# Kernel optimization log

Hardware: AMD Instinct MI355X
Metric: run time of the kernel (lower is better)

Reference implementation:

```python
import jax, jax.numpy as jnp
import numpy as np

HIDDEN, HEADS, HDIM = 1024, 8, 64
B, S = 4, 8192
LN_EPS = 1e-6


def setup_inputs() -> dict:
    key = jax.random.key(0)
    ks = jax.random.split(key, 12)
    inner = HEADS * HDIM
    sd = HIDDEN ** -0.5
    return {
        "x": jax.random.normal(ks[0], (B, S, HIDDEN), jnp.float32),
        "Wq": jax.random.normal(ks[1], (HIDDEN, inner), jnp.float32) * sd,
        "bq": jnp.zeros((inner,), jnp.float32),
        "Wk": jax.random.normal(ks[2], (HIDDEN, inner), jnp.float32) * sd,
        "bk": jnp.zeros((inner,), jnp.float32),
        "Wv": jax.random.normal(ks[3], (HIDDEN, inner), jnp.float32) * sd,
        "bv": jnp.zeros((inner,), jnp.float32),
        "Wo": jax.random.normal(ks[4], (inner, HIDDEN), jnp.float32) * (inner ** -0.5),
        "bo": jnp.zeros((HIDDEN,), jnp.float32),
        "alpha": jnp.ones((HEADS, HDIM), jnp.float32),
        "aug_param": jax.random.normal(ks[5], (1, HEADS, HDIM), jnp.float32),
        "ln_scale": jnp.ones((HIDDEN,), jnp.float32),
        "ln_bias": jnp.zeros((HIDDEN,), jnp.float32),
    }


def reference(x, Wq, bq, Wk, bk, Wv, bv, Wo, bo, alpha, aug_param, ln_scale, ln_bias):
    b, s, _ = x.shape
    h, d = alpha.shape
    scale = d ** -0.5
    q = (x @ Wq + bq).reshape(b, s, h, d)
    k = (x @ Wk + bk).reshape(b, s, h, d)
    v = (x @ Wv + bv).reshape(b, s, h, d)
    decay = jax.nn.sigmoid(alpha)  # (h, d)

    def step(state, qkv):
        q_t, k_t, v_t = qkv  # each (b, h, d)
        attn = jax.nn.softmax(jnp.einsum('bhd,bhd->bh', q_t, k_t) * scale, axis=-1)
        new_state = decay * state + (1.0 - decay) * attn[..., None] * v_t
        return new_state, new_state

    qs = jnp.moveaxis(q, 1, 0)  # (s, b, h, d)
    ks_ = jnp.moveaxis(k, 1, 0)
    vs = jnp.moveaxis(v, 1, 0)
    init = jnp.zeros((b, h, d), x.dtype)
    _, states = jax.lax.scan(step, init, (qs, ks_, vs))
    states = jnp.moveaxis(states, 0, 1)  # (b, s, h, d)

    aug = jax.nn.sigmoid(q * aug_param)  # aug_param (1,h,d) broadcasts over (b,s,h,d)
    out = (q * states + aug).reshape(b, s, h * d)
    out = out @ Wo + bo
    mean = jnp.mean(out, axis=-1, keepdims=True)
    var = jnp.var(out, axis=-1, keepdims=True)
    return (out - mean) * jax.lax.rsqrt(var + LN_EPS) * ln_scale + ln_bias
```

## Files before the change

kernel.cpp:

```cpp
#include <hip/hip_runtime.h>
#include <hip/hip_bf16.h>


#define HIDDEN 1024
#define HEADS 8
#define HDIM 64
#define INNER 512
#define BATCH 4
#define SEQ 8192
#define ROWS (BATCH*SEQ)
#define NCHUNK 128
#define CHLEN 64

typedef unsigned short u16;
typedef unsigned int u32;
typedef __attribute__((ext_vector_type(8))) short bf16x8;
typedef __attribute__((ext_vector_type(4))) float f32x4;

__device__ __forceinline__ float b2f(u16 u) { return __uint_as_float(((u32)u) << 16); }
__device__ __forceinline__ u16 f2b(float f) {
  u32 u = __float_as_uint(f);
  u32 r = u + 0x7fffu + ((u >> 16) & 1u);
  return (u16)(r >> 16);
}
__device__ __forceinline__ u32 pack2(float a, float b) {
  return (u32)f2b(a) | ((u32)f2b(b) << 16);
}

#define GLOAD_LDS16(gp, lp)                                                  \
  __builtin_amdgcn_global_load_lds(                                          \
      (const __attribute__((address_space(1))) u32*)(gp),                    \
      (__attribute__((address_space(3))) u32*)(lp), 16, 0, 0)

__global__ __launch_bounds__(256) void prep_x(const float* __restrict__ x,
                                              u16* __restrict__ xb) {
  size_t i = ((size_t)blockIdx.x * 256 + threadIdx.x) * 8;
  float4 a = *(const float4*)(x + i);
  float4 b = *(const float4*)(x + i + 4);
  uint4 w = {pack2(a.x, a.y), pack2(a.z, a.w), pack2(b.x, b.y), pack2(b.z, b.w)};
  *(uint4*)(xb + i) = w;
}

__global__ __launch_bounds__(256) void prep_w(
    const float* __restrict__ Wq, const float* __restrict__ Wk,
    const float* __restrict__ Wv, const float* __restrict__ Wo,
    const float* __restrict__ bq, const float* __restrict__ bk,
    const float* __restrict__ bv,
    u16* __restrict__ Wt, u16* __restrict__ Wot, float* __restrict__ bcat) {
  const int WELEM = HIDDEN * INNER;
  int idx = blockIdx.x * 256 + threadIdx.x;
  if (idx < 3 * WELEM) {
    int z = idx / WELEM;
    int rem = idx - z * WELEM;
    int n = rem >> 10;
    int k = rem & 1023;
    const float* W = (z == 0) ? Wq : (z == 1) ? Wk : Wv;
    Wt[idx] = f2b(W[k * INNER + n]);
  } else {
    int rem = idx - 3 * WELEM;
    int n = rem >> 9;
    int k = rem & 511;
    Wot[rem] = f2b(Wo[k * HIDDEN + n]);
  }
  if (idx < 3 * INNER) {
    int z = idx >> 9;
    int n = idx & 511;
    bcat[idx] = (z == 0) ? bq[n] : (z == 1) ? bk[n] : bv[n];
  }
}

template <int K, bool SPLIT3>
__global__ __launch_bounds__(512, 2) void gemm_8ph(
    const u16* __restrict__ A, const u16* __restrict__ Bt,
    const float* __restrict__ bias,
    void* __restrict__ out0, void* __restrict__ out1, void* __restrict__ out2,
    int nTilesN) {
  constexpr int NT = K / 32;
  __shared__ u16 lds[4][16384];

  const int nwg = gridDim.x;
  const int chunk = nwg >> 3;
  const int bid = blockIdx.x;
  const int lin = (bid & 7) * chunk + (bid >> 3);
  const int nt = lin % nTilesN;
  const int mt = lin / nTilesN;
  const int m0 = mt * 256, n0 = nt * 256;
  const int N = nTilesN * 256;

  const int tid = threadIdx.x;
  const int lane = tid & 63;
  const int w = tid >> 6;
  const int wm = w >> 2;
  const int wn = w & 3;
  const int r16 = lane & 15, kq = lane >> 4;

  const int rt = tid >> 2;
  const int cg = (((tid & 3) << 3)) ^ (((rt >> 1) & 3) << 3);
  const u16* Ag = A + (size_t)(m0 + rt) * K + cg;
  const u16* Bg = Bt + (size_t)(n0 + rt) * K + cg;
  const int ldst = w * 512;

#define STAGE_A(slot, kt)                                                     \
  {                                                                           \
    GLOAD_LDS16(Ag + (size_t)(kt) * 32, &lds[slot][ldst]);                    \
    GLOAD_LDS16(Ag + (size_t)(kt) * 32 + (size_t)128 * K,                     \
                &lds[slot][4096 + ldst]);                                     \
  }
#define STAGE_B(slot, kt)                                                     \
  {                                                                           \
    GLOAD_LDS16(Bg + (size_t)(kt) * 32, &lds[slot][8192 + ldst]);             \
    GLOAD_LDS16(Bg + (size_t)(kt) * 32 + (size_t)128 * K,                     \
                &lds[slot][12288 + ldst]);                                    \
  }

  const int xk = (kq << 3) ^ (((r16 >> 1) & 3) << 3);
  const int aO = (wm * 128 + r16) * 32 + xk;
  const int bO = 8192 + (wn * 64 + r16) * 32 + xk;

  f32x4 acc[8][4] = {};
  bf16x8 af[4], bfv[4];

#define PH0(t_, STG)                                                           \
  {                                                                            \
    const u16* sl = &lds[(t_) & 3][0];                                         \
    _Pragma("unroll") for (int i = 0; i < 4; i++)                              \
        af[i] = *(const bf16x8*)&sl[aO + i * 512];                             \
    _Pragma("unroll") for (int j = 0; j < 4; j++)                              \
        bfv[j] = *(const bf16x8*)&sl[bO + j * 512];                            \
    STG;                                                                       \
    __builtin_amdgcn_sched_barrier(0);                                         \
    __builtin_amdgcn_s_barrier();                                              \
    asm volatile("s_waitcnt lgkmcnt(0)" ::: "memory");                         \
    __builtin_amdgcn_sched_barrier(0);                                         \
    __builtin_amdgcn_s_setprio(1);                                             \
    _Pragma("unroll") for (int i = 0; i < 4; i++)                              \
        _Pragma("unroll") for (int j = 0; j < 4; j++)                          \
            acc[i][j] =                                                        \
        __builtin_amdgcn_mfma_f32_16x16x32_bf16(af[i], bfv[j], acc[i][j], 0, 0, 0); \
    __builtin_amdgcn_s_setprio(0);                                             \
    __builtin_amdgcn_sched_barrier(0);                                         \
    __builtin_amdgcn_s_barrier();                                              \
  }

#define PH1(t_, STG, VM)                                                       \
  {                                                                            \
    const u16* sl = &lds[(t_) & 3][0];                                         \
    _Pragma("unroll") for (int i = 0; i < 4; i++)                              \
        af[i] = *(const bf16x8*)&sl[aO + (i + 4) * 512];                       \
    STG;                                                                       \
    asm volatile("s_waitcnt vmcnt(" #VM ")" ::: "memory");                     \
    __builtin_amdgcn_sched_barrier(0);                                         \
    __builtin_amdgcn_s_barrier();                                              \
    asm volatile("s_waitcnt lgkmcnt(0)" ::: "memory");                         \
    __builtin_amdgcn_sched_barrier(0);                                         \
    __builtin_amdgcn_s_setprio(1);                                             \
    _Pragma("unroll") for (int i = 0; i < 4; i++)                              \
        _Pragma("unroll") for (int j = 0; j < 4; j++)                          \
            acc[i + 4][j] =                                                    \
        __builtin_amdgcn_mfma_f32_16x16x32_bf16(af[i], bfv[j], acc[i + 4][j], 0, 0, 0); \
    __builtin_amdgcn_s_setprio(0);                                             \
    __builtin_amdgcn_sched_barrier(0);                                         \
    __builtin_amdgcn_s_barrier();                                              \
  }

#define NOSTG ((void)0)

  STAGE_A(0, 0); STAGE_B(0, 0);
  STAGE_A(1, 1); STAGE_B(1, 1);
  STAGE_A(2, 2); STAGE_B(2, 2);
  asm volatile("s_waitcnt vmcnt(8)" ::: "memory");
  __builtin_amdgcn_sched_barrier(0);
  __builtin_amdgcn_s_barrier();

  for (int t = 0; t < NT - 3; ++t) {
    PH0(t, STAGE_A((t + 3) & 3, t + 3));
    PH1(t, STAGE_B((t + 3) & 3, t + 3), 8);
  }
  PH0(NT - 3, NOSTG);
  PH1(NT - 3, NOSTG, 4);
  PH0(NT - 2, NOSTG);
  PH1(NT - 2, NOSTG, 0);
  PH0(NT - 1, NOSTG);
  PH1(NT - 1, NOSTG, 0);
#undef PH0
#undef PH1
#undef NOSTG
#undef STAGE_A
#undef STAGE_B

  float* fl = (float*)(&lds[0][0]) + w * 4096;
  const int zsel = SPLIT3 ? ((n0 + wn * 64) >> 9) : 0;
  u16* ob = SPLIT3 ? (u16*)((zsel == 0) ? out0 : (zsel == 1) ? out1 : out2)
                   : (u16*)out0;
  const int OC = SPLIT3 ? INNER : N;
  const int colloc = (lane & 7) * 8;
  const int gcol = (SPLIT3 ? ((n0 + wn * 64) & 511) : (n0 + wn * 64)) + colloc;
  const int lrowr = lane >> 3;
  float bvj[4];
#pragma unroll
  for (int j = 0; j < 4; j++) bvj[j] = bias[n0 + wn * 64 + j * 16 + r16];

#pragma unroll
  for (int pass = 0; pass < 4; ++pass) {
#pragma unroll
    for (int ii = 0; ii < 2; ++ii) {
#pragma unroll
      for (int j = 0; j < 4; ++j) {
#pragma unroll
        for (int q = 0; q < 4; ++q)
          fl[(ii * 16 + kq * 4 + q) * 68 + j * 16 + r16] =
              acc[pass * 2 + ii][j][q] + bvj[j];
      }
    }
#pragma unroll
    for (int inst = 0; inst < 4; ++inst) {
      int lr = inst * 8 + lrowr;
      float4 f0 = *(float4*)&fl[lr * 68 + colloc];
      float4 f1 = *(float4*)&fl[lr * 68 + colloc + 4];
      uint4 wv = {pack2(f0.x, f0.y), pack2(f0.z, f0.w),
                  pack2(f1.x, f1.y), pack2(f1.z, f1.w)};
      size_t grow = (size_t)(m0 + wm * 128 + pass * 32 + lr);
      *(uint4*)&ob[grow * OC + gcol] = wv;
    }
  }
}

template <bool A_BF16>
__global__ __launch_bounds__(256) void gemm128(
    const void* __restrict__ Aany, const u16* __restrict__ BtBase,
    const float* __restrict__ bias0, const float* __restrict__ bias1,
    const float* __restrict__ bias2,
    void* __restrict__ out0, void* __restrict__ out1, void* __restrict__ out2,
    int K) {
  __shared__ u16 As[128 * 32];
  __shared__ u16 Bs[128 * 32];
  const int N = gridDim.x * 128;
  const int z = blockIdx.z;
  const u16* Bt = BtBase + (size_t)z * N * K;
  const float* bias = (z == 0) ? bias0 : (z == 1) ? bias1 : bias2;
  void* Out = (z == 0) ? out0 : (z == 1) ? out1 : out2;
  const int tid = threadIdx.x;
  const int m0 = blockIdx.y * 128;
  const int n0 = blockIdx.x * 128;
  const int lane = tid & 63;
  const int wid = tid >> 6;
  const int wm = wid >> 1, wn = wid & 1;
  const int r16 = lane & 15, kq = lane >> 4;
  const int r = tid >> 1;
  const int half = tid & 1;
  f32x4 acc[4][4] = {};
  for (int k0 = 0; k0 < K; k0 += 32) {
    __syncthreads();
    if (A_BF16) {
      const u16* Ab = (const u16*)Aany;
      const int4* src = (const int4*)(Ab + (size_t)(m0 + r) * K + k0 + half * 16);
      int4 v0 = src[0];
      int4 v1 = src[1];
      *(int4*)&As[r * 32 + half * 16] = v0;
      *(int4*)&As[r * 32 + half * 16 + 8] = v1;
    } else {
      const float* Af = (const float*)Aany;
      const float4* src = (const float4*)(Af + (size_t)(m0 + r) * K + k0 + half * 16);
      float4 f0 = src[0], f1 = src[1], f2 = src[2], f3 = src[3];
      uint4 w0 = {pack2(f0.x, f0.y), pack2(f0.z, f0.w), pack2(f1.x, f1.y), pack2(f1.z, f1.w)};
      uint4 w1 = {pack2(f2.x, f2.y), pack2(f2.z, f2.w), pack2(f3.x, f3.y), pack2(f3.z, f3.w)};
      *(uint4*)&As[r * 32 + half * 16] = w0;
      *(uint4*)&As[r * 32 + half * 16 + 8] = w1;
    }
    {
      const int4* src = (const int4*)(Bt + (size_t)(n0 + r) * K + k0 + half * 16);
      int4 v0 = src[0];
      int4 v1 = src[1];
      *(int4*)&Bs[r * 32 + half * 16] = v0;
      *(int4*)&Bs[r * 32 + half * 16 + 8] = v1;
    }
    __syncthreads();
    bf16x8 a[4], b[4];
#pragma unroll
    for (int i = 0; i < 4; i++)
      a[i] = *(const bf16x8*)&As[(wm * 64 + i * 16 + r16) * 32 + kq * 8];
#pragma unroll
    for (int j = 0; j < 4; j++)
      b[j] = *(const bf16x8*)&Bs[(wn * 64 + j * 16 + r16) * 32 + kq * 8];
#pragma unroll
    for (int i = 0; i < 4; i++)
#pragma unroll
      for (int j = 0; j < 4; j++)
        acc[i][j] = __builtin_amdgcn_mfma_f32_16x16x32_bf16(a[i], b[j], acc[i][j], 0, 0, 0);
  }
#pragma unroll
  for (int j = 0; j < 4; j++) {
    int col = n0 + wn * 64 + j * 16 + r16;
    float bv = bias[col];
#pragma unroll
    for (int i = 0; i < 4; i++) {
#pragma unroll
      for (int q = 0; q < 4; q++) {
        int row = m0 + wm * 64 + i * 16 + kq * 4 + q;
        float v = acc[i][j][q] + bv;
        ((u16*)Out)[(size_t)row * N + col] = f2b(v);
      }
    }
  }
}

__global__ __launch_bounds__(256) void attn_kernel(
    const u16* __restrict__ qb, const u16* __restrict__ kb,
    float* __restrict__ attn) {
  int lane = threadIdx.x & 63;
  int wid = threadIdx.x >> 6;
  size_t t = (size_t)blockIdx.x * 4 + wid;
  int4 qv = *(const int4*)(qb + t * INNER + lane * 8);
  int4 kv = *(const int4*)(kb + t * INNER + lane * 8);
  const u16* qu = (const u16*)&qv;
  const u16* ku = (const u16*)&kv;
  float s = 0.f;
#pragma unroll
  for (int j = 0; j < 8; j++) s += b2f(qu[j]) * b2f(ku[j]);
  s += __shfl_xor(s, 1);
  s += __shfl_xor(s, 2);
  s += __shfl_xor(s, 4);
  s *= 0.125f;
  float mx = s;
  mx = fmaxf(mx, __shfl_xor(mx, 8));
  mx = fmaxf(mx, __shfl_xor(mx, 16));
  mx = fmaxf(mx, __shfl_xor(mx, 32));
  float e = __expf(s - mx);
  float sm = e;
  sm += __shfl_xor(sm, 8);
  sm += __shfl_xor(sm, 16);
  sm += __shfl_xor(sm, 32);
  float a = e / sm;
  if ((lane & 7) == 0) attn[t * HEADS + (lane >> 3)] = a;
}

__global__ __launch_bounds__(512) void scan_phase1(
    const u16* __restrict__ vb, const float* __restrict__ attn,
    const float* __restrict__ alpha, float* __restrict__ ends) {
  int hd = threadIdx.x;
  int h = hd >> 6;
  int c = blockIdx.x, b = blockIdx.y;
  float decay = 1.f / (1.f + __expf(-alpha[hd]));
  float om = 1.f - decay;
  size_t base = (size_t)b * SEQ + (size_t)c * CHLEN;
  float st = 0.f;
#pragma unroll 8
  for (int i = 0; i < CHLEN; i++) {
    size_t t = base + i;
    float a = attn[t * HEADS + h];
    float v = b2f(vb[t * INNER + hd]);
    st = decay * st + om * a * v;
  }
  ends[((size_t)b * NCHUNK + c) * INNER + hd] = st;
}

__global__ __launch_bounds__(512) void scan_phase2(
    const float* __restrict__ ends, const float* __restrict__ alpha,
    float* __restrict__ carries) {
  int hd = threadIdx.x;
  int b = blockIdx.x;
  float decay = 1.f / (1.f + __expf(-alpha[hd]));
  float dL = __powf(decay, (float)CHLEN);
  float carry = 0.f;
#pragma unroll 8
  for (int c = 0; c < NCHUNK; c++) {
    size_t idx = ((size_t)b * NCHUNK + c) * INNER + hd;
    carries[idx] = carry;
    carry = dL * carry + ends[idx];
  }
}

__global__ __launch_bounds__(512) void scan_phase3(
    const u16* __restrict__ qb, const u16* __restrict__ vb,
    const float* __restrict__ attn, const float* __restrict__ alpha,
    const float* __restrict__ augp, const float* __restrict__ carries,
    u16* __restrict__ outpre) {
  int hd = threadIdx.x;
  int h = hd >> 6;
  int c = blockIdx.x, b = blockIdx.y;
  float decay = 1.f / (1.f + __expf(-alpha[hd]));
  float om = 1.f - decay;
  float ap = augp[hd];
  float st = carries[((size_t)b * NCHUNK + c) * INNER + hd];
  size_t base = (size_t)b * SEQ + (size_t)c * CHLEN;
#pragma unroll 4
  for (int i = 0; i < CHLEN; i++) {
    size_t t = base + i;
    float a = attn[t * HEADS + h];
    float v = b2f(vb[t * INNER + hd]);
    st = decay * st + om * a * v;
    float q = b2f(qb[t * INNER + hd]);
    float aug = 1.f / (1.f + __expf(-q * ap));
    outpre[t * INNER + hd] = f2b(q * st + aug);
  }
}

__global__ __launch_bounds__(256) void ln_kernel(
    const u16* __restrict__ outln, float* __restrict__ out,
    const float* __restrict__ lns, const float* __restrict__ lnb) {
  size_t row = blockIdx.x;
  int tid = threadIdx.x;
  uint2 rv = *(const uint2*)(outln + row * HIDDEN + tid * 4);
  const u16* p = (const u16*)&rv;
  float v0 = b2f(p[0]), v1 = b2f(p[1]), v2 = b2f(p[2]), v3 = b2f(p[3]);
  float s = v0 + v1 + v2 + v3;
  float ss = v0 * v0 + v1 * v1 + v2 * v2 + v3 * v3;
#pragma unroll
  for (int m = 1; m < 64; m <<= 1) {
    s += __shfl_xor(s, m);
    ss += __shfl_xor(ss, m);
  }
  __shared__ float sb[4], ssb[4];
  int lane = tid & 63, wid = tid >> 6;
  if (lane == 0) {
    sb[wid] = s;
    ssb[wid] = ss;
  }
  __syncthreads();
  s = sb[0] + sb[1] + sb[2] + sb[3];
  ss = ssb[0] + ssb[1] + ssb[2] + ssb[3];
  float mean = s * (1.f / HIDDEN);
  float var = ss * (1.f / HIDDEN) - mean * mean;
  float rstd = rsqrtf(var + 1e-6f);
  float4 sc = *(const float4*)(lns + tid * 4);
  float4 bi = *(const float4*)(lnb + tid * 4);
  float4 o;
  o.x = (v0 - mean) * rstd * sc.x + bi.x;
  o.y = (v1 - mean) * rstd * sc.y + bi.y;
  o.z = (v2 - mean) * rstd * sc.z + bi.z;
  o.w = (v3 - mean) * rstd * sc.w + bi.w;
  *(float4*)(out + row * HIDDEN + tid * 4) = o;
}

extern "C" void kernel_launch(void* const* d_in, const int* in_sizes, int n_in,
                              void* d_out, int out_size, void* d_ws, size_t ws_size,
                              hipStream_t stream) {
  const float* x = (const float*)d_in[0];
  const float* Wq = (const float*)d_in[1];
  const float* bq = (const float*)d_in[2];
  const float* Wk = (const float*)d_in[3];
  const float* bk = (const float*)d_in[4];
  const float* Wv = (const float*)d_in[5];
  const float* bv = (const float*)d_in[6];
  const float* Wo = (const float*)d_in[7];
  const float* bo = (const float*)d_in[8];
  const float* alpha = (const float*)d_in[9];
  const float* augp = (const float*)d_in[10];
  const float* lns = (const float*)d_in[11];
  const float* lnb = (const float*)d_in[12];

  char* ws = (char*)d_ws;
  const bool fast = ws_size >= 175118336ull;

  if (fast) {
    u16* xb = (u16*)(ws + 0);
    u16* qb = (u16*)(ws + 67108864);
    u16* kb = (u16*)(ws + 100663296);
    u16* vb = (u16*)(ws + 134217728);
    u16* Wt = (u16*)(ws + 167772160);
    u16* Wot = (u16*)(ws + 170917888);
    float* bcat = (float*)(ws + 171966464);
    float* attn = (float*)(ws + 171972608);
    float* ends = (float*)(ws + 173021184);
    float* car = (float*)(ws + 174069760);
    u16* outpre = kb;
    u16* outln = xb;

    prep_x<<<ROWS * HIDDEN / 8 / 256, 256, 0, stream>>>(x, xb);
    prep_w<<<8192, 256, 0, stream>>>(Wq, Wk, Wv, Wo, bq, bk, bv, Wt, Wot, bcat);

    gemm_8ph<HIDDEN, true><<<768, 512, 0, stream>>>(
        xb, Wt, bcat, qb, kb, vb, 6);

    attn_kernel<<<ROWS / 4, 256, 0, stream>>>(qb, kb, attn);
    scan_phase1<<<dim3(NCHUNK, BATCH), 512, 0, stream>>>(vb, attn, alpha, ends);
    scan_phase2<<<BATCH, 512, 0, stream>>>(ends, alpha, car);
    scan_phase3<<<dim3(NCHUNK, BATCH), 512, 0, stream>>>(qb, vb, attn, alpha, augp, car, outpre);

    gemm_8ph<INNER, false><<<512, 512, 0, stream>>>(
        outpre, Wot, bo, outln, outln, outln, 4);

    ln_kernel<<<ROWS, 256, 0, stream>>>(outln, (float*)d_out, lns, lnb);
  } else {
    u16* qb = (u16*)(ws + 0);
    u16* vb = (u16*)(ws + 33554432);
    u16* kb = (u16*)(ws + 67108864);
    u16* Wt = (u16*)(ws + 100663296);
    u16* Wot = (u16*)(ws + 103809024);
    float* bcat = (float*)(ws + 104845312);
    float* attn = (float*)(ws + 104857600);
    float* ends = (float*)(ws + 105906176);
    float* car = (float*)(ws + 106954752);
    u16* outpre = kb;
    u16* outln = (u16*)(ws + 0);

    prep_w<<<8192, 256, 0, stream>>>(Wq, Wk, Wv, Wo, bq, bk, bv, Wt, Wot, bcat);
    gemm128<false><<<dim3(4, 256, 3), 256, 0, stream>>>(
        x, Wt, bq, bk, bv, qb, kb, vb, HIDDEN);
    attn_kernel<<<ROWS / 4, 256, 0, stream>>>(qb, kb, attn);
    scan_phase1<<<dim3(NCHUNK, BATCH), 512, 0, stream>>>(vb, attn, alpha, ends);
    scan_phase2<<<BATCH, 512, 0, stream>>>(ends, alpha, car);
    scan_phase3<<<dim3(NCHUNK, BATCH), 512, 0, stream>>>(qb, vb, attn, alpha, augp, car, outpre);
    gemm_8ph<INNER, false><<<512, 512, 0, stream>>>(
        outpre, Wot, bo, outln, outln, outln, 4);
    ln_kernel<<<ROWS, 256, 0, stream>>>(outln, (float*)d_out, lns, lnb);
  }
}
```

Before: 278.8 us.

## Merge two GEMM K-step phases into one tile step with a single barrier

Replaces the two-phase per-K-tile loop (each phase with two workgroup barriers and its own LDS reads) with one TILE step. It issues both A and B stage loads up front, reads all A and B fragments, runs 32 MFMAs, then waits on vmcnt and hits one barrier. This cuts barriers per K-tile from four to one and lets the compiler overlap LDS reads with MFMAs. In exchange it holds more fragment registers live (af0, af1, bfv4), and it drops the explicit lgkmcnt waits, so correctness now depends on compiler-inserted waits and on the 4-slot ring leaving enough distance to avoid LDS overwrite races.

```diff
diff --git a/kernel.cpp b/kernel.cpp
--- a/kernel.cpp
+++ b/kernel.cpp
@@ -100,14 +100,11 @@
   const u16* Bg = Bt + (size_t)(n0 + rt) * K + cg;
   const int ldst = w * 512;
 
-#define STAGE_A(slot, kt)                                                     \
+#define STAGE_AB(slot, kt)                                                    \
   {                                                                           \
     GLOAD_LDS16(Ag + (size_t)(kt) * 32, &lds[slot][ldst]);                    \
     GLOAD_LDS16(Ag + (size_t)(kt) * 32 + (size_t)128 * K,                     \
                 &lds[slot][4096 + ldst]);                                     \
-  }
-#define STAGE_B(slot, kt)                                                     \
-  {                                                                           \
     GLOAD_LDS16(Bg + (size_t)(kt) * 32, &lds[slot][8192 + ldst]);             \
     GLOAD_LDS16(Bg + (size_t)(kt) * 32 + (size_t)128 * K,                     \
                 &lds[slot][12288 + ldst]);                                    \
@@ -118,75 +115,64 @@
   const int bO = 8192 + (wn * 64 + r16) * 32 + xk;
 
   f32x4 acc[8][4] = {};
-  bf16x8 af[4], bfv[4];
-
-#define PH0(t_, STG)                                                           \
+
+#define TILE(t_, STG, VMW)                                                     \
   {                                                                            \
+    STG;                                                                       \
     const u16* sl = &lds[(t_) & 3][0];                                         \
+    bf16x8 af0[4], af1[4], bfv4[4];                                            \
     _Pragma("unroll") for (int i = 0; i < 4; i++)                              \
-        af[i] = *(const bf16x8*)&sl[aO + i * 512];                             \
+        af0[i] = *(const bf16x8*)&sl[aO + i * 512];                            \
     _Pragma("unroll") for (int j = 0; j < 4; j++)                              \
-        bfv[j] = *(const bf16x8*)&sl[bO + j * 512];                            \
-    STG;                                                                       \
+        bfv4[j] = *(const bf16x8*)&sl[bO + j * 512];                           \
     __builtin_amdgcn_sched_barrier(0);                                         \
-    __builtin_amdgcn_s_barrier();                                              \
-    asm volatile("s_waitcnt lgkmcnt(0)" ::: "memory");                         \
+    _Pragma("unroll") for (int i = 0; i < 4; i++)                              \
+        af1[i] = *(const bf16x8*)&sl[aO + (i + 4) * 512];                      \
     __builtin_amdgcn_sched_barrier(0);                                         \
     __builtin_amdgcn_s_setprio(1);                                             \
     _Pragma("unroll") for (int i = 0; i < 4; i++)                              \
         _Pragma("unroll") for (int j = 0; j < 4; j++)                          \
             acc[i][j] =                                                        \
-        __builtin_amdgcn_mfma_f32_16x16x32_bf16(af[i], bfv[j], acc[i][j], 0, 0, 0); \
+        __builtin_amdgcn_mfma_f32_16x16x32_bf16(af0[i], bfv4[j], acc[i][j], 0, 0, 0); \
     __builtin_amdgcn_s_setprio(0);                                             \
-    __builtin_amdgcn_sched_barrier(0);                                         \
-    __builtin_amdgcn_s_barrier();                                              \
-  }
-
-#define PH1(t_, STG, VM)                                                       \
-  {                                                                            \
-    const u16* sl = &lds[(t_) & 3][0];                                         \
-    _Pragma("unroll") for (int i = 0; i < 4; i++)                              \
-        af[i] = *(const bf16x8*)&sl[aO + (i + 4) * 512];                       \
-    STG;                                                                       \
-    asm volatile("s_waitcnt vmcnt(" #VM ")" ::: "memory");                     \
-    __builtin_amdgcn_sched_barrier(0);                                         \
-    __builtin_amdgcn_s_barrier();                                              \
-    asm volatile("s_waitcnt lgkmcnt(0)" ::: "memory");                         \
     __builtin_amdgcn_sched_barrier(0);                                         \
     __builtin_amdgcn_s_setprio(1);                                             \
     _Pragma("unroll") for (int i = 0; i < 4; i++)                              \
         _Pragma("unroll") for (int j = 0; j < 4; j++)                          \
             acc[i + 4][j] =                                                    \
-        __builtin_amdgcn_mfma_f32_16x16x32_bf16(af[i], bfv[j], acc[i + 4][j], 0, 0, 0); \
+        __builtin_amdgcn_mfma_f32_16x16x32_bf16(af1[i], bfv4[j], acc[i + 4][j], 0, 0, 0); \
     __builtin_amdgcn_s_setprio(0);                                             \
+    VMW;                                                                       \
     __builtin_amdgcn_sched_barrier(0);                                         \
     __builtin_amdgcn_s_barrier();                                              \
   }
 
+#define VM8 asm volatile("s_waitcnt vmcnt(8)" ::: "memory")
+#define VM4 asm volatile("s_waitcnt vmcnt(4)" ::: "memory")
+#define VM0 asm volatile("s_waitcnt vmcnt(0)" ::: "memory")
 #define NOSTG ((void)0)
-
-  STAGE_A(0, 0); STAGE_B(0, 0);
-  STAGE_A(1, 1); STAGE_B(1, 1);
-  STAGE_A(2, 2); STAGE_B(2, 2);
-  asm volatile("s_waitcnt vmcnt(8)" ::: "memory");
+#define NOVM ((void)0)
+
+  STAGE_AB(0, 0);
+  STAGE_AB(1, 1);
+  STAGE_AB(2, 2);
+  VM8;
   __builtin_amdgcn_sched_barrier(0);
   __builtin_amdgcn_s_barrier();
 
   for (int t = 0; t < NT - 3; ++t) {
-    PH0(t, STAGE_A((t + 3) & 3, t + 3));
-    PH1(t, STAGE_B((t + 3) & 3, t + 3), 8);
-  }
-  PH0(NT - 3, NOSTG);
-  PH1(NT - 3, NOSTG, 4);
-  PH0(NT - 2, NOSTG);
-  PH1(NT - 2, NOSTG, 0);
-  PH0(NT - 1, NOSTG);
-  PH1(NT - 1, NOSTG, 0);
-#undef PH0
-#undef PH1
+    TILE(t, STAGE_AB((t + 3) & 3, t + 3), VM8);
+  }
+  TILE(NT - 3, NOSTG, VM4);
+  TILE(NT - 2, NOSTG, VM0);
+  TILE(NT - 1, NOSTG, NOVM);
+#undef TILE
+#undef STAGE_AB
+#undef VM8
+#undef VM4
+#undef VM0
 #undef NOSTG
-#undef STAGE_A
-#undef STAGE_B
+#undef NOVM
 
   float* fl = (float*)(&lds[0][0]) + w * 4096;
   const int zsel = SPLIT3 ? ((n0 + wn * 64) >> 9) : 0;
```

Result: no change. 275.1 us (-1.3%).
